# Optimization experiments

Hardware: AMD Instinct MI355X
Metric: run time of the kernel (lower is better)

## Reference

```python
import jax, jax.numpy as jnp
import numpy as np

EPS = 1e-5

def _conv(x, w, pad):
    # NCHW / OIHW 2-D convolution, stride 1
    return jax.lax.conv_general_dilated(
        x, w, window_strides=(1, 1), padding=[(pad, pad), (pad, pad)],
        dimension_numbers=('NCHW', 'OIHW', 'NCHW'))

def _bn2d(x, g, b, m, v):
    inv = g * jax.lax.rsqrt(v + EPS)
    return x * inv[None, :, None, None] + (b - m * inv)[None, :, None, None]

def _bn1d(x, g, b, m, v):
    inv = g * jax.lax.rsqrt(v + EPS)
    return x * inv[None, :] + (b - m * inv)[None, :]

def _avgpool2(x):
    B, C, H, W = x.shape
    return x.reshape(B, C, H // 2, 2, W // 2, 2).mean(axis=(3, 5))

def _hardtanh01(x):
    return jnp.clip(x, 0.0, 1.0)

def setup_inputs() -> dict:
    key = jax.random.key(0)
    ks = jax.random.split(key, 24)
    B = 1024
    d = {}
    d['x_in'] = jax.random.normal(ks[0], (B, 3, 32, 32), dtype=jnp.float32)
    d['w1'] = jax.random.normal(ks[1], (32, 3, 5, 5), dtype=jnp.float32) * 0.1
    d['w2'] = jax.random.normal(ks[2], (32, 32, 5, 5), dtype=jnp.float32) * 0.05
    d['w3'] = jax.random.normal(ks[3], (64, 32, 5, 5), dtype=jnp.float32) * 0.05
    d['w4'] = jax.random.normal(ks[4], (10, 64, 4, 4), dtype=jnp.float32) * 0.05
    for i, (c, k0) in enumerate([(32, 5), (32, 9), (64, 13), (10, 17)], start=1):
        d[f'g{i}'] = jax.random.uniform(ks[k0], (c,), minval=0.5, maxval=1.5, dtype=jnp.float32)
        d[f'b{i}'] = jax.random.normal(ks[k0 + 1], (c,), dtype=jnp.float32) * 0.1
        d[f'm{i}'] = jax.random.normal(ks[k0 + 2], (c,), dtype=jnp.float32) * 0.1
        d[f'v{i}'] = jax.random.uniform(ks[k0 + 3], (c,), minval=0.5, maxval=1.5, dtype=jnp.float32)
    return d

def reference(x_in, w1, w2, w3, w4,
              g1, b1, m1, v1, g2, b2, m2, v2,
              g3, b3, m3, v3, g4, b4, m4, v4):
    # conv1 -> bn1 -> pool -> hardtanh(0,1)
    x = _hardtanh01(_avgpool2(_bn2d(_conv(x_in, w1, 2), g1, b1, m1, v1)))
    # conv2 -> bn2 -> pool -> hardtanh(0,1)
    x = _hardtanh01(_avgpool2(_bn2d(_conv(x, w2, 2), g2, b2, m2, v2)))
    # conv3 -> bn3 -> pool -> hardtanh(0,1)
    x = _hardtanh01(_avgpool2(_bn2d(_conv(x, w3, 2), g3, b3, m3, v3)))
    # fc1 as 4x4 conv, valid padding -> (B, num_classes, 1, 1)
    x = _conv(x, w4, 0).reshape(x.shape[0], -1)
    return _bn1d(x, g4, b4, m4, v4)
```

## Files before the change

kernel.cpp:

```cpp
#include <hip/hip_runtime.h>

#define EPSF 1e-5f

typedef _Float16 half8 __attribute__((ext_vector_type(8)));
typedef float f32x4 __attribute__((ext_vector_type(4)));

__device__ __forceinline__ float clamp01(float x){ return fminf(fmaxf(x, 0.f), 1.f); }

__global__ __launch_bounds__(256) void k_prep(
    const float* __restrict__ w1, const float* __restrict__ w2,
    const float* __restrict__ w3, const float* __restrict__ w4,
    const float* __restrict__ g1, const float* __restrict__ b1, const float* __restrict__ m1, const float* __restrict__ v1,
    const float* __restrict__ g2, const float* __restrict__ b2, const float* __restrict__ m2, const float* __restrict__ v2,
    const float* __restrict__ g3, const float* __restrict__ b3, const float* __restrict__ m3, const float* __restrict__ v3,
    const float* __restrict__ g4, const float* __restrict__ b4, const float* __restrict__ m4, const float* __restrict__ v4,
    _Float16* __restrict__ w1e, _Float16* __restrict__ w2e, _Float16* __restrict__ w3e,
    _Float16* __restrict__ w4h, float* __restrict__ bnc)
{
  const int t = blockIdx.x*256 + threadIdx.x;
  if (t < 6144) {
    int c = t / 192, k = t - c*192;
    int oc = (c < 16) ? 2*c : 2*(c-16)+1;
    int u = k >> 5, rem = k & 31, v = rem >> 2, ic = rem & 3;
    float val = 0.f;
    if (v < 6 && ic < 3) {
      #pragma unroll
      for (int r = 0; r < 2; ++r)
        #pragma unroll
        for (int cc = 0; cc < 2; ++cc) {
          int uu = u - r, vv = v - cc;
          if ((unsigned)uu < 5u && (unsigned)vv < 5u)
            val += w1[(oc*3+ic)*25 + uu*5 + vv];
        }
    }
    w1e[t] = (_Float16)val;
  }
  for (int i = t; i < 36864; i += 32768) {
    int tap = i >> 10, r2 = i & 1023, c = r2 >> 5, ic = r2 & 31;
    int oc = (c < 16) ? 2*c : 2*(c-16)+1;
    int u = tap / 6, v = tap - u*6;
    float val = 0.f;
    #pragma unroll
    for (int r = 0; r < 2; ++r)
      #pragma unroll
      for (int cc = 0; cc < 2; ++cc) {
        int uu = u - r, vv = v - cc;
        if ((unsigned)uu < 5u && (unsigned)vv < 5u)
          val += w2[(oc*32+ic)*25 + uu*5 + vv];
      }
    w2e[i] = (_Float16)val;
  }
  for (int i = t; i < 73728; i += 32768) {
    int tap = i >> 11, r2 = i & 2047, oc = r2 >> 5, ic = r2 & 31;
    int u = tap / 6, v = tap - u*6;
    float val = 0.f;
    #pragma unroll
    for (int r = 0; r < 2; ++r)
      #pragma unroll
      for (int cc = 0; cc < 2; ++cc) {
        int uu = u - r, vv = v - cc;
        if ((unsigned)uu < 5u && (unsigned)vv < 5u)
          val += w3[(oc*32+ic)*25 + uu*5 + vv];
      }
    w3e[i] = (_Float16)val;
  }
  for (int i = t; i < 16384; i += 32768) {
    int oc = i >> 10, k = i & 1023, pos = k >> 6, ic = k & 63;
    float val = (oc < 10) ? w4[(oc*64+ic)*16 + pos] : 0.f;
    w4h[i] = (_Float16)val;
  }
  if (t < 32) {
    float inv = g1[t] / sqrtf(v1[t] + EPSF);
    bnc[t] = 0.25f*inv; bnc[32+t] = b1[t] - m1[t]*inv;
    float i2 = g2[t] / sqrtf(v2[t] + EPSF);
    bnc[64+t] = 0.25f*i2; bnc[96+t] = b2[t] - m2[t]*i2;
  }
  if (t < 64) {
    float i3 = g3[t] / sqrtf(v3[t] + EPSF);
    bnc[128+t] = 0.25f*i3; bnc[192+t] = b3[t] - m3[t]*i3;
  }
  if (t < 10) {
    float i4 = g4[t] / sqrtf(v4[t] + EPSF);
    bnc[256+t] = i4; bnc[266+t] = b4[t] - m4[t]*i4;
  }
}

__global__ __launch_bounds__(512, 6) void k_fused(
    const float* __restrict__ x,
    const _Float16* __restrict__ w1e, const _Float16* __restrict__ w2e,
    const _Float16* __restrict__ w3e, const _Float16* __restrict__ w4h,
    const float* __restrict__ bnc, float* __restrict__ out)
{
  __shared__ __align__(16) char arena[32000];
  _Float16* Pimg = (_Float16*)arena;
  _Float16* P2   = (_Float16*)arena;
  _Float16* P3   = (_Float16*)arena;
  _Float16* Ip3  = (_Float16*)(arena + 11520);
  float*    S4P  = (float*)(arena + 13568);

  const int img = blockIdx.x;
  const int tid = threadIdx.x;
  const int w   = __builtin_amdgcn_readfirstlane(tid >> 6);
  const int l   = tid & 63;
  const int row = l & 15;
  const int kg  = l >> 4;
  const int mtb = w & 3;
  const int ntb = w >> 2;

  for (int i = tid; i < 720; i += 512)
    ((float4*)arena)[i] = make_float4(0.f,0.f,0.f,0.f);
  __syncthreads();

  {
    const float* xin = x + img*3072;
    for (int i = tid; i < 768; i += 512) {
      int ic = i >> 8, rem = i & 255;
      int y = rem >> 3, xq = rem & 7;
      float4 v4 = *(const float4*)(xin + ic*1024 + y*32 + xq*4);
      _Float16* dst = Pimg + (y+2)*160 + (xq*4 + 2)*4 + ic;
      dst[0]  = (_Float16)v4.x; dst[4]  = (_Float16)v4.y;
      dst[8]  = (_Float16)v4.z; dst[12] = (_Float16)v4.w;
    }
  }
  __syncthreads();

  f32x4 acc1[4];
  {
    half8 B1[6];
    #pragma unroll
    for (int u = 0; u < 6; ++u)
      B1[u] = *(const half8*)(w1e + (ntb*16 + row)*192 + u*32 + kg*8);
    #pragma unroll
    for (int t2 = 0; t2 < 4; ++t2) acc1[t2] = (f32x4){0,0,0,0};
    const int xoff = 8*(row + kg);
    #pragma unroll
    for (int t2 = 0; t2 < 4; ++t2) {
      const int py = mtb*4 + t2;
      #pragma unroll
      for (int u = 0; u < 6; ++u) {
        half8 av = *(const half8*)(Pimg + (2*py + u)*160 + xoff);
        acc1[t2] = __builtin_amdgcn_mfma_f32_16x16x32_f16(av, B1[u], acc1[t2], 0, 0, 0);
      }
    }
  }
  __syncthreads();

  for (int j = tid; j < 1600; j += 512) {
    int u = j & 3, pos = j >> 2;
    int a = pos/20, c = pos - a*20;
    bool interior = ((unsigned)(a-2) < 16u) & ((unsigned)(c-2) < 16u);
    if (!interior) *(half8*)(P2 + pos*40 + u*8) = (half8)(_Float16)0.f;
  }
  {
    const int oc = 2*row + ntb;
    const float sA = bnc[oc], hA = bnc[32 + oc];
    #pragma unroll
    for (int t2 = 0; t2 < 4; ++t2) {
      const int py = mtb*4 + t2;
      #pragma unroll
      for (int r = 0; r < 4; ++r) {
        int px = kg*4 + r;
        P2[((py+2)*20 + px+2)*40 + oc] = (_Float16)clamp01(fmaf(acc1[t2][r], sA, hA));
      }
    }
  }
  __syncthreads();

  f32x4 a2 = {0,0,0,0};
  {
    const int pixel = mtb*16 + row;
    const int py = pixel >> 3, px = pixel & 7;
    const _Float16* base = P2 + (2*py)*800 + (2*px)*40 + kg*8;
    const _Float16* wb = w2e + (ntb*16 + row)*32 + kg*8;
    half8 wreg[4];
    #pragma unroll
    for (int q = 0; q < 4; ++q) wreg[q] = *(const half8*)(wb + q*1024);
    #pragma unroll
    for (int u = 0; u < 6; ++u)
      #pragma unroll
      for (int v = 0; v < 6; ++v) {
        const int tap = u*6 + v;
        const int tn = (tap < 32) ? tap + 4 : tap;
        half8 nw = *(const half8*)(wb + tn*1024);
        half8 av = *(const half8*)(base + u*800 + v*40);
        a2 = __builtin_amdgcn_mfma_f32_16x16x32_f16(av, wreg[tap & 3], a2, 0, 0, 0);
        wreg[tap & 3] = nw;
      }
  }
  __syncthreads();

  for (int j = tid; j < 576; j += 512) {
    int u = j & 3, pos = j >> 2;
    int a = pos/12, c = pos - a*12;
    bool interior = ((unsigned)(a-2) < 8u) & ((unsigned)(c-2) < 8u);
    if (!interior) *(half8*)(P3 + pos*40 + u*8) = (half8)(_Float16)0.f;
  }
  {
    const int oc = 2*row + ntb;
    const float sA = bnc[64 + oc], hA = bnc[96 + oc];
    #pragma unroll
    for (int r = 0; r < 4; ++r) {
      int p2 = mtb*16 + kg*4 + r;
      int py2 = p2 >> 3, px2 = p2 & 7;
      P3[((py2+2)*12 + px2+2)*40 + oc] = (_Float16)clamp01(fmaf(a2[r], sA, hA));
    }
  }
  __syncthreads();

  if (w < 4) {
    const int py = row >> 2, px = row & 3;
    const _Float16* base = P3 + (2*py)*480 + (2*px)*40 + kg*8;
    const _Float16* wb = w3e + (w*16 + row)*32 + kg*8;
    half8 wreg[4];
    #pragma unroll
    for (int q = 0; q < 4; ++q) wreg[q] = *(const half8*)(wb + q*2048);
    f32x4 a3 = {0,0,0,0};
    #pragma unroll
    for (int u = 0; u < 6; ++u)
      #pragma unroll
      for (int v = 0; v < 6; ++v) {
        const int tap = u*6 + v;
        const int tn = (tap < 32) ? tap + 4 : tap;
        half8 nw = *(const half8*)(wb + tn*2048);
        half8 av = *(const half8*)(base + u*480 + v*40);
        a3 = __builtin_amdgcn_mfma_f32_16x16x32_f16(av, wreg[tap & 3], a3, 0, 0, 0);
        wreg[tap & 3] = nw;
      }
    const int oc = w*16 + row;
    const float s3 = bnc[128 + oc], h3 = bnc[192 + oc];
    #pragma unroll
    for (int r = 0; r < 4; ++r)
      Ip3[(kg*4 + r)*64 + oc] = (_Float16)clamp01(fmaf(a3[r], s3, h3));
  }
  __syncthreads();

  if (tid < 160) {
    const int oc = tid >> 4, pix = tid & 15;
    const _Float16* A = Ip3 + pix*64;
    const _Float16* W = w4h + oc*1024 + pix*64;
    float a = 0.f;
    #pragma unroll
    for (int q = 0; q < 8; ++q) {
      half8 xa = *(const half8*)(A + q*8);
      half8 wv = *(const half8*)(W + q*8);
      #pragma unroll
      for (int j = 0; j < 8; ++j)
        a = fmaf((float)xa[j], (float)wv[j], a);
    }
    S4P[tid] = a;
  }
  __syncthreads();
  if (tid < 10) {
    float s = 0.f;
    #pragma unroll
    for (int i = 0; i < 16; ++i) s += S4P[tid*16 + i];
    out[img*10 + tid] = fmaf(s, bnc[256 + tid], bnc[266 + tid]);
  }
}

extern "C" void kernel_launch(void* const* d_in, const int* in_sizes, int n_in,
                              void* d_out, int out_size, void* d_ws, size_t ws_size,
                              hipStream_t stream)
{
  const float* x  = (const float*)d_in[0];
  const float* w1 = (const float*)d_in[1];
  const float* w2 = (const float*)d_in[2];
  const float* w3 = (const float*)d_in[3];
  const float* w4 = (const float*)d_in[4];
  const float *g1=(const float*)d_in[5],  *b1=(const float*)d_in[6],
              *m1=(const float*)d_in[7],  *v1=(const float*)d_in[8];
  const float *g2=(const float*)d_in[9],  *b2=(const float*)d_in[10],
              *m2=(const float*)d_in[11], *v2=(const float*)d_in[12];
  const float *g3=(const float*)d_in[13], *b3=(const float*)d_in[14],
              *m3=(const float*)d_in[15], *v3=(const float*)d_in[16];
  const float *g4=(const float*)d_in[17], *b4=(const float*)d_in[18],
              *m4=(const float*)d_in[19], *v4=(const float*)d_in[20];
  float* out = (float*)d_out;

  char* ws = (char*)d_ws;
  _Float16* w1e = (_Float16*)(ws);
  _Float16* w2e = (_Float16*)(ws + 12288);
  _Float16* w3e = (_Float16*)(ws + 86016);
  _Float16* w4h = (_Float16*)(ws + 233472);
  float*    bnc = (float*)   (ws + 266240);

  k_prep<<<dim3(128), dim3(256), 0, stream>>>(w1, w2, w3, w4,
      g1,b1,m1,v1, g2,b2,m2,v2, g3,b3,m3,v3, g4,b4,m4,v4,
      w1e, w2e, w3e, w4h, bnc);
  k_fused<<<dim3(1024), dim3(512), 0, stream>>>(x, w1e, w2e, w3e, w4h, bnc, out);
}
```

Measured before the change: 135.3 us.

## Process two images per block to reuse weight registers across images

Each workgroup now handles two images instead of one. Conv1 and conv2 weight fragments loaded into registers are reused for two MFMAs each, and conv3 now keeps all 8 waves busy (4 per image) instead of only 4. Shared memory per block doubles to 64000 bytes and the launch bound drops to 4 waves per SIMD. Only 512 blocks are launched, which lowers occupancy and halves the number of blocks available to fill the 256 CUs.

After: 126.3 us. -6.7%, faster.

```diff
diff --git a/kernel.cpp b/kernel.cpp
--- a/kernel.cpp
+++ b/kernel.cpp
@@ -85,20 +85,20 @@
   }
 }
 
-__global__ __launch_bounds__(512, 6) void k_fused(
+__global__ __launch_bounds__(512, 4) void k_fused(
     const float* __restrict__ x,
     const _Float16* __restrict__ w1e, const _Float16* __restrict__ w2e,
     const _Float16* __restrict__ w3e, const _Float16* __restrict__ w4h,
     const float* __restrict__ bnc, float* __restrict__ out)
 {
-  __shared__ __align__(16) char arena[32000];
+  __shared__ __align__(16) char arena[64000];
   _Float16* Pimg = (_Float16*)arena;
   _Float16* P2   = (_Float16*)arena;
   _Float16* P3   = (_Float16*)arena;
-  _Float16* Ip3  = (_Float16*)(arena + 11520);
-  float*    S4P  = (float*)(arena + 13568);
-
-  const int img = blockIdx.x;
+  _Float16* Ip3  = (_Float16*)(arena + 23040);
+  float*    S4P  = (float*)(arena + 27136);
+
+  const int i0  = blockIdx.x * 2;
   const int tid = threadIdx.x;
   const int w   = __builtin_amdgcn_readfirstlane(tid >> 6);
   const int l   = tid & 63;
@@ -107,66 +107,74 @@
   const int mtb = w & 3;
   const int ntb = w >> 2;
 
-  for (int i = tid; i < 720; i += 512)
+  for (int i = tid; i < 1440; i += 512)
     ((float4*)arena)[i] = make_float4(0.f,0.f,0.f,0.f);
   __syncthreads();
 
-  {
-    const float* xin = x + img*3072;
-    for (int i = tid; i < 768; i += 512) {
-      int ic = i >> 8, rem = i & 255;
-      int y = rem >> 3, xq = rem & 7;
-      float4 v4 = *(const float4*)(xin + ic*1024 + y*32 + xq*4);
-      _Float16* dst = Pimg + (y+2)*160 + (xq*4 + 2)*4 + ic;
-      dst[0]  = (_Float16)v4.x; dst[4]  = (_Float16)v4.y;
-      dst[8]  = (_Float16)v4.z; dst[12] = (_Float16)v4.w;
-    }
-  }
-  __syncthreads();
-
-  f32x4 acc1[4];
+  for (int i = tid; i < 1536; i += 512) {
+    int im = i / 768, rem2 = i - im*768;
+    int ic = rem2 >> 8, rem = rem2 & 255;
+    int y = rem >> 3, xq = rem & 7;
+    float4 v4 = *(const float4*)(x + (i0+im)*3072 + ic*1024 + y*32 + xq*4);
+    _Float16* dst = Pimg + im*5760 + (y+2)*160 + (xq*4 + 2)*4 + ic;
+    dst[0]  = (_Float16)v4.x; dst[4]  = (_Float16)v4.y;
+    dst[8]  = (_Float16)v4.z; dst[12] = (_Float16)v4.w;
+  }
+  __syncthreads();
+
+  f32x4 acc1[2][4];
   {
     half8 B1[6];
     #pragma unroll
     for (int u = 0; u < 6; ++u)
       B1[u] = *(const half8*)(w1e + (ntb*16 + row)*192 + u*32 + kg*8);
     #pragma unroll
-    for (int t2 = 0; t2 < 4; ++t2) acc1[t2] = (f32x4){0,0,0,0};
+    for (int im = 0; im < 2; ++im)
+      #pragma unroll
+      for (int t2 = 0; t2 < 4; ++t2) acc1[im][t2] = (f32x4){0,0,0,0};
     const int xoff = 8*(row + kg);
     #pragma unroll
     for (int t2 = 0; t2 < 4; ++t2) {
       const int py = mtb*4 + t2;
       #pragma unroll
       for (int u = 0; u < 6; ++u) {
-        half8 av = *(const half8*)(Pimg + (2*py + u)*160 + xoff);
-        acc1[t2] = __builtin_amdgcn_mfma_f32_16x16x32_f16(av, B1[u], acc1[t2], 0, 0, 0);
+        const int ro = (2*py + u)*160 + xoff;
+        half8 a0 = *(const half8*)(Pimg + ro);
+        half8 a1 = *(const half8*)(Pimg + 5760 + ro);
+        acc1[0][t2] = __builtin_amdgcn_mfma_f32_16x16x32_f16(a0, B1[u], acc1[0][t2], 0, 0, 0);
+        acc1[1][t2] = __builtin_amdgcn_mfma_f32_16x16x32_f16(a1, B1[u], acc1[1][t2], 0, 0, 0);
       }
     }
   }
   __syncthreads();
 
-  for (int j = tid; j < 1600; j += 512) {
-    int u = j & 3, pos = j >> 2;
+  for (int j = tid; j < 3200; j += 512) {
+    int im = j / 1600, jj = j - im*1600;
+    int u = jj & 3, pos = jj >> 2;
     int a = pos/20, c = pos - a*20;
     bool interior = ((unsigned)(a-2) < 16u) & ((unsigned)(c-2) < 16u);
-    if (!interior) *(half8*)(P2 + pos*40 + u*8) = (half8)(_Float16)0.f;
+    if (!interior) *(half8*)(P2 + im*16000 + pos*40 + u*8) = (half8)(_Float16)0.f;
   }
   {
     const int oc = 2*row + ntb;
     const float sA = bnc[oc], hA = bnc[32 + oc];
     #pragma unroll
-    for (int t2 = 0; t2 < 4; ++t2) {
-      const int py = mtb*4 + t2;
-      #pragma unroll
-      for (int r = 0; r < 4; ++r) {
-        int px = kg*4 + r;
-        P2[((py+2)*20 + px+2)*40 + oc] = (_Float16)clamp01(fmaf(acc1[t2][r], sA, hA));
-      }
-    }
-  }
-  __syncthreads();
-
-  f32x4 a2 = {0,0,0,0};
+    for (int im = 0; im < 2; ++im)
+      #pragma unroll
+      for (int t2 = 0; t2 < 4; ++t2) {
+        const int py = mtb*4 + t2;
+        #pragma unroll
+        for (int r = 0; r < 4; ++r) {
+          int px = kg*4 + r;
+          P2[im*16000 + ((py+2)*20 + px+2)*40 + oc] =
+              (_Float16)clamp01(fmaf(acc1[im][t2][r], sA, hA));
+        }
+      }
+  }
+  __syncthreads();
+
+  f32x4 a2[2];
+  a2[0] = (f32x4){0,0,0,0}; a2[1] = (f32x4){0,0,0,0};
   {
     const int pixel = mtb*16 + row;
     const int py = pixel >> 3, px = pixel & 7;
@@ -182,35 +190,43 @@
         const int tap = u*6 + v;
         const int tn = (tap < 32) ? tap + 4 : tap;
         half8 nw = *(const half8*)(wb + tn*1024);
-        half8 av = *(const half8*)(base + u*800 + v*40);
-        a2 = __builtin_amdgcn_mfma_f32_16x16x32_f16(av, wreg[tap & 3], a2, 0, 0, 0);
+        const int ro = u*800 + v*40;
+        half8 av0 = *(const half8*)(base + ro);
+        half8 av1 = *(const half8*)(base + 16000 + ro);
+        a2[0] = __builtin_amdgcn_mfma_f32_16x16x32_f16(av0, wreg[tap & 3], a2[0], 0, 0, 0);
+        a2[1] = __builtin_amdgcn_mfma_f32_16x16x32_f16(av1, wreg[tap & 3], a2[1], 0, 0, 0);
         wreg[tap & 3] = nw;
       }
   }
   __syncthreads();
 
-  for (int j = tid; j < 576; j += 512) {
-    int u = j & 3, pos = j >> 2;
+  for (int j = tid; j < 1152; j += 512) {
+    int im = j / 576, jj = j - im*576;
+    int u = jj & 3, pos = jj >> 2;
     int a = pos/12, c = pos - a*12;
     bool interior = ((unsigned)(a-2) < 8u) & ((unsigned)(c-2) < 8u);
-    if (!interior) *(half8*)(P3 + pos*40 + u*8) = (half8)(_Float16)0.f;
+    if (!interior) *(half8*)(P3 + im*5760 + pos*40 + u*8) = (half8)(_Float16)0.f;
   }
   {
     const int oc = 2*row + ntb;
     const float sA = bnc[64 + oc], hA = bnc[96 + oc];
     #pragma unroll
-    for (int r = 0; r < 4; ++r) {
-      int p2 = mtb*16 + kg*4 + r;
-      int py2 = p2 >> 3, px2 = p2 & 7;
-      P3[((py2+2)*12 + px2+2)*40 + oc] = (_Float16)clamp01(fmaf(a2[r], sA, hA));
-    }
-  }
-  __syncthreads();
-
-  if (w < 4) {
+    for (int im = 0; im < 2; ++im)
+      #pragma unroll
+      for (int r = 0; r < 4; ++r) {
+        int p2 = mtb*16 + kg*4 + r;
+        int py2 = p2 >> 3, px2 = p2 & 7;
+        P3[im*5760 + ((py2+2)*12 + px2+2)*40 + oc] =
+            (_Float16)clamp01(fmaf(a2[im][r], sA, hA));
+      }
+  }
+  __syncthreads();
+
+  {
+    const int im = w >> 2, nt = w & 3;
     const int py = row >> 2, px = row & 3;
-    const _Float16* base = P3 + (2*py)*480 + (2*px)*40 + kg*8;
-    const _Float16* wb = w3e + (w*16 + row)*32 + kg*8;
+    const _Float16* base = P3 + im*5760 + (2*py)*480 + (2*px)*40 + kg*8;
+    const _Float16* wb = w3e + (nt*16 + row)*32 + kg*8;
     half8 wreg[4];
     #pragma unroll
     for (int q = 0; q < 4; ++q) wreg[q] = *(const half8*)(wb + q*2048);
@@ -226,17 +242,18 @@
         a3 = __builtin_amdgcn_mfma_f32_16x16x32_f16(av, wreg[tap & 3], a3, 0, 0, 0);
         wreg[tap & 3] = nw;
       }
-    const int oc = w*16 + row;
+    const int oc = nt*16 + row;
     const float s3 = bnc[128 + oc], h3 = bnc[192 + oc];
     #pragma unroll
     for (int r = 0; r < 4; ++r)
-      Ip3[(kg*4 + r)*64 + oc] = (_Float16)clamp01(fmaf(a3[r], s3, h3));
-  }
-  __syncthreads();
-
-  if (tid < 160) {
-    const int oc = tid >> 4, pix = tid & 15;
-    const _Float16* A = Ip3 + pix*64;
+      Ip3[im*1024 + (kg*4 + r)*64 + oc] = (_Float16)clamp01(fmaf(a3[r], s3, h3));
+  }
+  __syncthreads();
+
+  if (tid < 320) {
+    const int im = tid / 160, t2 = tid - im*160;
+    const int oc = t2 >> 4, pix = t2 & 15;
+    const _Float16* A = Ip3 + im*1024 + pix*64;
     const _Float16* W = w4h + oc*1024 + pix*64;
     float a = 0.f;
     #pragma unroll
@@ -247,14 +264,15 @@
       for (int j = 0; j < 8; ++j)
         a = fmaf((float)xa[j], (float)wv[j], a);
     }
-    S4P[tid] = a;
-  }
-  __syncthreads();
-  if (tid < 10) {
+    S4P[im*160 + t2] = a;
+  }
+  __syncthreads();
+  if (tid < 20) {
+    const int im = tid / 10, oc = tid - im*10;
     float s = 0.f;
     #pragma unroll
-    for (int i = 0; i < 16; ++i) s += S4P[tid*16 + i];
-    out[img*10 + tid] = fmaf(s, bnc[256 + tid], bnc[266 + tid]);
+    for (int i = 0; i < 16; ++i) s += S4P[im*160 + oc*16 + i];
+    out[(i0+im)*10 + oc] = fmaf(s, bnc[256 + oc], bnc[266 + oc]);
   }
 }
 
@@ -287,5 +305,5 @@
   k_prep<<<dim3(128), dim3(256), 0, stream>>>(w1, w2, w3, w4,
       g1,b1,m1,v1, g2,b2,m2,v2, g3,b3,m3,v3, g4,b4,m4,v4,
       w1e, w2e, w3e, w4h, bnc);
-  k_fused<<<dim3(1024), dim3(512), 0, stream>>>(x, w1e, w2e, w3e, w4h, bnc, out);
+  k_fused<<<dim3(512), dim3(512), 0, stream>>>(x, w1e, w2e, w3e, w4h, bnc, out);
 }
```
